# Kernel optimization log

Hardware: AMD Instinct MI355X
Metric: run time of the kernel (lower is better)

## Reference

```python
import jax, jax.numpy as jnp
import numpy as np

B, D, H, M, N, S = 256, 256, 512, 64, 2048, 3
SHIFTS = (1, 0, -1)  # = range(S//2, -S//2, -1); matches np.roll(eye, s, axis=1) one-hot matrices


def setup_inputs():
    key = jax.random.key(0)
    k = jax.random.split(key, 24)
    f32 = jnp.float32

    def rn(i, shape, scale):
        return jax.random.normal(k[i], shape, f32) * scale

    rh = jax.random.uniform(k[3], (B, N), f32)
    wh = jax.random.uniform(k[4], (B, N), f32)
    sc_ih = 1.0 / np.sqrt(D + M)
    sc_h = 1.0 / np.sqrt(H)
    return dict(
        inp=rn(0, (B, D), 1.0),
        h_tm1=rn(1, (B, H), 0.1),
        c_tm1=rn(2, (B, H), 0.1),
        read_head_tm1=rh / rh.sum(1, keepdims=True),
        write_head_tm1=wh / wh.sum(1, keepdims=True),
        memory=rn(5, (B, N, M), 0.5),
        W_ih=rn(6, (4 * H, D + M), sc_ih), W_hh=rn(7, (4 * H, H), sc_h),
        b_ih=jnp.zeros((4 * H,), f32), b_hh=jnp.zeros((4 * H,), f32),
        W_rk=rn(8, (M, H), sc_h), b_rk=rn(9, (M,), 0.01),
        W_wk=rn(10, (M, H), sc_h), b_wk=rn(11, (M,), 0.01),
        W_rc=rn(12, (3, H), sc_h), b_rc=jnp.zeros((3,), f32),
        W_wc=rn(13, (3, H), sc_h), b_wc=jnp.zeros((3,), f32),
        W_rs=rn(14, (S, H), sc_h), b_rs=jnp.zeros((S,), f32),
        W_ws=rn(15, (S, H), sc_h), b_ws=jnp.zeros((S,), f32),
        W_w=rn(16, (2 * M, H), sc_h), b_w=jnp.zeros((2 * M,), f32),
    )


def _head_params(h, Wk, bk, Wc, bc, Ws, bs):
    kk = jnp.tanh(h @ Wk.T + bk)                     # [B,M] key
    c = h @ Wc.T + bc                                # [B,3]
    beta = jax.nn.relu(c[:, 0:1]) + 1e-4             # focus strength
    g = jax.nn.sigmoid(c[:, 1:2])                    # interpolation gate
    gamma = jax.nn.relu(c[:, 2:3]) + 1.0001          # sharpening power
    s = jax.nn.softmax(h @ Ws.T + bs, axis=1)        # [B,S] shift weights
    return kk, s, beta, g, gamma


def _address(memory, head_tm1, kk, s, beta, g, gamma):
    dot = jnp.einsum('bm,bnm->bn', kk, memory)
    nk = jnp.linalg.norm(kk, axis=1, keepdims=True)  # [B,1]
    nM = jnp.linalg.norm(memory, axis=2)             # [B,N]
    cos = dot / jnp.maximum(nk * nM, 1e-8)
    content = jax.nn.softmax(beta * cos, axis=1)
    inter = g * content + (1.0 - g) * head_tm1       # gated interpolation [B,N]
    # circular shift; identical math to contracting with the one-hot C tensor
    rolled = jnp.stack([jnp.roll(inter, -sh, axis=1) for sh in SHIFTS], axis=1)  # [B,S,N]
    out = jnp.einsum('bsn,bs->bn', rolled, s)
    out = out ** gamma                               # sharpen
    return out / out.sum(1, keepdims=True)


def reference(inp, h_tm1, c_tm1, read_head_tm1, write_head_tm1, memory,
              W_ih, W_hh, b_ih, b_hh, W_rk, b_rk, W_wk, b_wk,
              W_rc, b_rc, W_wc, b_wc, W_rs, b_rs, W_ws, b_ws, W_w, b_w):
    # read addressing uses previous hidden state
    rp = _head_params(h_tm1, W_rk, b_rk, W_rc, b_rc, W_rs, b_rs)
    read_head = _address(memory, read_head_tm1, *rp)
    M_read = jnp.einsum('bn,bnm->bm', read_head, memory)  # [B,M]
    # LSTMCell controller (torch gate order i,f,g,o)
    x = jnp.concatenate([inp, M_read], axis=1)
    z = x @ W_ih.T + b_ih + h_tm1 @ W_hh.T + b_hh
    zi, zf, zg, zo = jnp.split(z, 4, axis=1)
    c_t = jax.nn.sigmoid(zf) * c_tm1 + jax.nn.sigmoid(zi) * jnp.tanh(zg)
    h_t = jax.nn.sigmoid(zo) * jnp.tanh(c_t)
    # write addressing uses new hidden state
    wp = _head_params(h_t, W_wk, b_wk, W_wc, b_wc, W_ws, b_ws)
    write_head = _address(memory, write_head_tm1, *wp)
    wa = h_t @ W_w.T + b_w
    e = jax.nn.sigmoid(wa[:, :M])                    # erase
    a = jnp.tanh(wa[:, M:])                          # add
    ww = write_head[:, :, None]                      # [B,N,1]
    M_out = memory * (1.0 - ww * e[:, None, :]) + ww * a[:, None, :]
    return (h_t, c_t, read_head, write_head, M_out)
```

## Files before the change

### kernel.cpp

```cpp
#include <hip/hip_runtime.h>
#include <hip/hip_bf16.h>

#define Bb 256
#define Dd 256
#define Hh 512
#define Mm 64
#define Nn 2048

typedef __attribute__((ext_vector_type(8))) short bf16x8;
typedef __attribute__((ext_vector_type(4))) float f32x4;

static __device__ __forceinline__ short f2bf(float f) {
    unsigned u = __float_as_uint(f);
    unsigned r = (u + 0x7FFFu + ((u >> 16) & 1u)) >> 16;
    return (short)r;
}

__global__ __launch_bounds__(256) void head_params_kernel(
    const float* __restrict__ h,
    const float* __restrict__ Wk, const float* __restrict__ bk,
    const float* __restrict__ Wc, const float* __restrict__ bc,
    const float* __restrict__ Ws, const float* __restrict__ bs,
    float* __restrict__ kk, float* __restrict__ par)
{
    int b = blockIdx.x;
    __shared__ float hs[Hh];
    __shared__ float red[6];
    __shared__ float skk[Mm];
    const float* hb = h + (size_t)b * Hh;
    for (int i = threadIdx.x; i < Hh; i += 256) hs[i] = hb[i];
    __syncthreads();

    int m   = threadIdx.x >> 2;
    int sub = threadIdx.x & 3;
    {
        const float* w = Wk + (size_t)m * Hh + sub * 128;
        const float* hh = hs + sub * 128;
        float acc = 0.f;
        #pragma unroll 8
        for (int k = 0; k < 128; ++k) acc += hh[k] * w[k];
        acc += __shfl_xor(acc, 1, 64);
        acc += __shfl_xor(acc, 2, 64);
        if (sub == 0) {
            float v = tanhf(acc + bk[m]);
            kk[(size_t)b * Mm + m] = v;
            skk[m] = v;
        }
    }
    if (threadIdx.x < 24) {
        int o  = threadIdx.x >> 2;
        int su = threadIdx.x & 3;
        const float* w = ((o < 3) ? (Wc + (size_t)o * Hh) : (Ws + (size_t)(o - 3) * Hh)) + su * 128;
        const float* hh = hs + su * 128;
        float acc = 0.f;
        #pragma unroll 8
        for (int k = 0; k < 128; ++k) acc += hh[k] * w[k];
        acc += __shfl_xor(acc, 1, 64);
        acc += __shfl_xor(acc, 2, 64);
        if (su == 0) red[o] = acc + ((o < 3) ? bc[o] : bs[o - 3]);
    }
    __syncthreads();
    if (threadIdx.x == 0) {
        float beta  = fmaxf(red[0], 0.f) + 1e-4f;
        float g     = 1.f / (1.f + __expf(-red[1]));
        float gamma = fmaxf(red[2], 0.f) + 1.0001f;
        float l0 = red[3], l1 = red[4], l2 = red[5];
        float mx = fmaxf(l0, fmaxf(l1, l2));
        float e0 = __expf(l0 - mx), e1 = __expf(l1 - mx), e2 = __expf(l2 - mx);
        float inv = 1.f / (e0 + e1 + e2);
        float ssq = 0.f;
        #pragma unroll
        for (int i = 0; i < Mm; ++i) ssq += skk[i] * skk[i];
        float* p = par + (size_t)b * 8;
        p[0] = beta; p[1] = g; p[2] = gamma;
        p[3] = e0 * inv; p[4] = e1 * inv; p[5] = e2 * inv;
        p[6] = sqrtf(ssq);
    }
}

__global__ __launch_bounds__(1024) void wparams_wvec_kernel(
    const float* __restrict__ h,
    const float* __restrict__ Wk, const float* __restrict__ bk,
    const float* __restrict__ Wc, const float* __restrict__ bc,
    const float* __restrict__ Ws, const float* __restrict__ bs,
    const float* __restrict__ W_w, const float* __restrict__ b_w,
    float* __restrict__ kk, float* __restrict__ par, float* __restrict__ ea)
{
    int b = blockIdx.x;
    int t = threadIdx.x;
    __shared__ float hs[Hh];
    __shared__ float red6[6];
    __shared__ float skk[Mm];
    if (t < Hh) hs[t] = h[(size_t)b * Hh + t];
    __syncthreads();
    if (t < 256) {
        int m = t >> 2, sub = t & 3;
        const float* w = Wk + (size_t)m * Hh + sub * 128;
        const float* hh = hs + sub * 128;
        float acc = 0.f;
        #pragma unroll 8
        for (int k = 0; k < 128; ++k) acc += hh[k] * w[k];
        acc += __shfl_xor(acc, 1, 64);
        acc += __shfl_xor(acc, 2, 64);
        if (sub == 0) {
            float v = tanhf(acc + bk[m]);
            skk[m] = v;
            kk[(size_t)b * Mm + m] = v;
        }
    } else if (t < 280) {
        int o = (t - 256) >> 2, su = t & 3;
        const float* w = ((o < 3) ? (Wc + (size_t)o * Hh) : (Ws + (size_t)(o - 3) * Hh)) + su * 128;
        const float* hh = hs + su * 128;
        float acc = 0.f;
        #pragma unroll 8
        for (int k = 0; k < 128; ++k) acc += hh[k] * w[k];
        acc += __shfl_xor(acc, 1, 64);
        acc += __shfl_xor(acc, 2, 64);
        if (su == 0) red6[o] = acc + ((o < 3) ? bc[o] : bs[o - 3]);
    } else if (t >= 512) {
        int o = (t - 512) >> 2, su = t & 3;
        const float* w = W_w + (size_t)o * Hh + su * 128;
        const float* hh = hs + su * 128;
        float acc = 0.f;
        #pragma unroll 8
        for (int k = 0; k < 128; ++k) acc += hh[k] * w[k];
        acc += __shfl_xor(acc, 1, 64);
        acc += __shfl_xor(acc, 2, 64);
        if (su == 0) {
            float v = acc + b_w[o];
            ea[(size_t)b * 128 + o] = (o < Mm) ? (1.f / (1.f + __expf(-v))) : tanhf(v);
        }
    }
    __syncthreads();
    if (t < 64) {
        float v = skk[t];
        float ssq = v * v;
        #pragma unroll
        for (int msk = 1; msk < 64; msk <<= 1) ssq += __shfl_xor(ssq, msk, 64);
        if (t == 0) {
            float beta  = fmaxf(red6[0], 0.f) + 1e-4f;
            float g     = 1.f / (1.f + __expf(-red6[1]));
            float gamma = fmaxf(red6[2], 0.f) + 1.0001f;
            float l0 = red6[3], l1 = red6[4], l2 = red6[5];
            float mx = fmaxf(l0, fmaxf(l1, l2));
            float e0 = __expf(l0 - mx), e1 = __expf(l1 - mx), e2 = __expf(l2 - mx);
            float inv = 1.f / (e0 + e1 + e2);
            float* p = par + (size_t)b * 8;
            p[0] = beta; p[1] = g; p[2] = gamma;
            p[3] = e0 * inv; p[4] = e1 * inv; p[5] = e2 * inv;
            p[6] = sqrtf(ssq);
        }
    }
}

template <int COMPUTE_NORM>
__global__ __launch_bounds__(256) void cos_pass_kernel(
    const float* __restrict__ mem, const float* __restrict__ kk,
    const float* __restrict__ par, float* __restrict__ cosv,
    float* __restrict__ nM)
{
    int b  = blockIdx.x >> 3;
    int n0 = (blockIdx.x & 7) << 8;
    int w  = threadIdx.x >> 6;
    int l  = threadIdx.x & 63;
    int m4 = l & 15;
    int rq = l >> 4;

    float4 kv = ((const float4*)(kk + (size_t)b * Mm))[m4];
    float kn = par[(size_t)b * 8 + 6];
    const float4* mb4 = (const float4*)(mem + (size_t)b * Nn * Mm);

    #pragma unroll
    for (int q = 0; q < 16; ++q) {
        int n = n0 + w * 64 + q * 4 + rq;
        size_t row = (size_t)b * Nn + n;
        float4 v = mb4[(size_t)n * 16 + m4];
        float dot = v.x * kv.x + v.y * kv.y + v.z * kv.z + v.w * kv.w;
        dot += __shfl_xor(dot, 1, 64);
        dot += __shfl_xor(dot, 2, 64);
        dot += __shfl_xor(dot, 4, 64);
        dot += __shfl_xor(dot, 8, 64);
        if (COMPUTE_NORM) {
            float ss = v.x * v.x + v.y * v.y + v.z * v.z + v.w * v.w;
            ss += __shfl_xor(ss, 1, 64);
            ss += __shfl_xor(ss, 2, 64);
            ss += __shfl_xor(ss, 4, 64);
            ss += __shfl_xor(ss, 8, 64);
            if (m4 == 0) {
                float nm = sqrtf(ss);
                nM[row] = nm;
                cosv[row] = dot / fmaxf(kn * nm, 1e-8f);
            }
        } else {
            if (m4 == 0) {
                float nm = nM[row];
                cosv[row] = dot / fmaxf(kn * nm, 1e-8f);
            }
        }
    }
}

__global__ __launch_bounds__(1024) void raddr_mread_kernel(
    const float* __restrict__ cosv, const float* __restrict__ par,
    const float* __restrict__ prev, const float* __restrict__ mem,
    float* __restrict__ outh, float* __restrict__ mrd)
{
    int b = blockIdx.x;
    int t = threadIdx.x;
    int w = t >> 6, l = t & 63;
    __shared__ float csh[Nn];
    __shared__ float redw[16];
    __shared__ float4 red4[64][16];

    const float* pv = par + (size_t)b * 8;
    float beta = pv[0], g = pv[1], gamma = pv[2];
    float s0 = pv[3], s1 = pv[4], s2 = pv[5];

    float v0 = beta * cosv[(size_t)b * Nn + t];
    float v1 = beta * cosv[(size_t)b * Nn + t + 1024];
    float mx = fmaxf(v0, v1);
    #pragma unroll
    for (int msk = 1; msk < 64; msk <<= 1) mx = fmaxf(mx, __shfl_xor(mx, msk, 64));
    if (l == 0) redw[w] = mx;
    __syncthreads();
    mx = redw[0];
    #pragma unroll
    for (int i = 1; i < 16; ++i) mx = fmaxf(mx, redw[i]);
    float e0 = __expf(v0 - mx), e1 = __expf(v1 - mx);
    float sum = e0 + e1;
    #pragma unroll
    for (int msk = 1; msk < 64; msk <<= 1) sum += __shfl_xor(sum, msk, 64);
    __syncthreads();
    if (l == 0) redw[w] = sum;
    __syncthreads();
    sum = 0.f;
    #pragma unroll
    for (int i = 0; i < 16; ++i) sum += redw[i];
    float invs = 1.f / sum;
    const float* pb = prev + (size_t)b * Nn;
    float i0 = g * e0 * invs + (1.f - g) * pb[t];
    float i1 = g * e1 * invs + (1.f - g) * pb[t + 1024];
    csh[t] = i0; csh[t + 1024] = i1;
    __syncthreads();
    int n1 = t + 1024;
    float c0 = s0 * csh[(t + 1) & (Nn - 1)] + s1 * i0 + s2 * csh[(t - 1) & (Nn - 1)];
    float c1 = s0 * csh[(n1 + 1) & (Nn - 1)] + s1 * i1 + s2 * csh[(n1 - 1) & (Nn - 1)];
    float p0 = exp2f(gamma * __log2f(c0));
    float p1 = exp2f(gamma * __log2f(c1));
    float osum = p0 + p1;
    #pragma unroll
    for (int msk = 1; msk < 64; msk <<= 1) osum += __shfl_xor(osum, msk, 64);
    __syncthreads();
    if (l == 0) redw[w] = osum;
    __syncthreads();
    osum = 0.f;
    #pragma unroll
    for (int i = 0; i < 16; ++i) osum += redw[i];
    float inv2 = 1.f / osum;
    float h0 = p0 * inv2, h1 = p1 * inv2;
    outh[(size_t)b * Nn + t] = h0;
    outh[(size_t)b * Nn + n1] = h1;
    __syncthreads();
    csh[t] = h0; csh[n1] = h1;
    __syncthreads();

    int r = t >> 4;
    int c = t & 15;
    const float4* mb4 = (const float4*)(mem + (size_t)b * Nn * Mm);
    float ax = 0.f, ay = 0.f, az = 0.f, aw = 0.f;
    for (int n = r; n < Nn; n += 64) {
        float wgt = csh[n];
        float4 v = mb4[(size_t)n * 16 + c];
        ax += wgt * v.x; ay += wgt * v.y; az += wgt * v.z; aw += wgt * v.w;
    }
    red4[r][c] = make_float4(ax, ay, az, aw);
    __syncthreads();
    if (t < 256) {
        int gg = t >> 4, cc = t & 15;
        float4 a = red4[gg * 4 + 0][cc], bq = red4[gg * 4 + 1][cc];
        float4 cv = red4[gg * 4 + 2][cc], d = red4[gg * 4 + 3][cc];
        red4[gg * 4][cc] = make_float4(a.x + bq.x + cv.x + d.x, a.y + bq.y + cv.y + d.y,
                                       a.z + bq.z + cv.z + d.z, a.w + bq.w + cv.w + d.w);
    }
    __syncthreads();
    if (t < 16) {
        float sx = 0.f, sy = 0.f, sz = 0.f, sw = 0.f;
        #pragma unroll
        for (int gg = 0; gg < 16; ++gg) {
            float4 v = red4[gg * 4][t];
            sx += v.x; sy += v.y; sz += v.z; sw += v.w;
        }
        ((float4*)(mrd + (size_t)b * Mm))[t] = make_float4(sx, sy, sz, sw);
    }
}

__global__ __launch_bounds__(256) void waddr_kernel(
    const float* __restrict__ cosv, const float* __restrict__ par,
    const float* __restrict__ prev, float* __restrict__ outh)
{
    int b = blockIdx.x;
    __shared__ float sh[Nn];
    __shared__ float red[4];
    const float* cb = cosv + (size_t)b * Nn;
    const float* pv = par + (size_t)b * 8;
    float beta = pv[0], g = pv[1], gamma = pv[2];
    float s0 = pv[3], s1 = pv[4], s2 = pv[5];
    int tid = threadIdx.x;

    float vals[8];
    float mx = -1e30f;
    #pragma unroll
    for (int i = 0; i < 8; ++i) {
        float v = beta * cb[tid + i * 256];
        vals[i] = v;
        mx = fmaxf(mx, v);
    }
    #pragma unroll
    for (int msk = 1; msk < 64; msk <<= 1) mx = fmaxf(mx, __shfl_xor(mx, msk, 64));
    if ((tid & 63) == 0) red[tid >> 6] = mx;
    __syncthreads();
    mx = fmaxf(fmaxf(red[0], red[1]), fmaxf(red[2], red[3]));

    float sum = 0.f;
    #pragma unroll
    for (int i = 0; i < 8; ++i) {
        float e = __expf(vals[i] - mx);
        vals[i] = e;
        sum += e;
    }
    #pragma unroll
    for (int msk = 1; msk < 64; msk <<= 1) sum += __shfl_xor(sum, msk, 64);
    __syncthreads();
    if ((tid & 63) == 0) red[tid >> 6] = sum;
    __syncthreads();
    sum = red[0] + red[1] + red[2] + red[3];
    float invs = 1.f / sum;

    const float* pb = prev + (size_t)b * Nn;
    #pragma unroll
    for (int i = 0; i < 8; ++i) {
        int n = tid + i * 256;
        sh[n] = g * vals[i] * invs + (1.f - g) * pb[n];
    }
    __syncthreads();

    float outs[8];
    float osum = 0.f;
    #pragma unroll
    for (int i = 0; i < 8; ++i) {
        int n = tid + i * 256;
        float v = s0 * sh[(n + 1) & (Nn - 1)] + s1 * sh[n] + s2 * sh[(n - 1) & (Nn - 1)];
        v = exp2f(gamma * __log2f(v));
        outs[i] = v;
        osum += v;
    }
    #pragma unroll
    for (int msk = 1; msk < 64; msk <<= 1) osum += __shfl_xor(osum, msk, 64);
    __syncthreads();
    if ((tid & 63) == 0) red[tid >> 6] = osum;
    __syncthreads();
    osum = red[0] + red[1] + red[2] + red[3];
    float inv2 = 1.f / osum;
    #pragma unroll
    for (int i = 0; i < 8; ++i)
        outh[(size_t)b * Nn + tid + i * 256] = outs[i] * inv2;
}

__global__ __launch_bounds__(256) void convW_kernel(
    const float* __restrict__ W_ih, const float* __restrict__ W_hh,
    short* __restrict__ Wb)
{
    unsigned g = blockIdx.x * 256 + threadIdx.x;
    unsigned j = g / 104u;
    unsigned kq = (g - j * 104u) * 8u;
    const float* src = (kq < 320u) ? (W_ih + (size_t)j * 320 + kq)
                                   : (W_hh + (size_t)j * 512 + (kq - 320u));
    float4 a = ((const float4*)src)[0];
    float4 c = ((const float4*)src)[1];
    bf16x8 o;
    o[0] = f2bf(a.x); o[1] = f2bf(a.y); o[2] = f2bf(a.z); o[3] = f2bf(a.w);
    o[4] = f2bf(c.x); o[5] = f2bf(c.y); o[6] = f2bf(c.z); o[7] = f2bf(c.w);
    *(bf16x8*)(Wb + (size_t)j * 832 + kq) = o;
}

__global__ __launch_bounds__(256) void convA_kernel(
    const float* __restrict__ inp, const float* __restrict__ mrd,
    const float* __restrict__ h, short* __restrict__ Ab)
{
    unsigned g = blockIdx.x * 256 + threadIdx.x;
    unsigned r = g / 104u;
    unsigned kq = (g - r * 104u) * 8u;
    const float* src;
    if (kq < 256u)      src = inp + (size_t)r * 256 + kq;
    else if (kq < 320u) src = mrd + (size_t)r * 64 + (kq - 256u);
    else                src = h + (size_t)r * 512 + (kq - 320u);
    float4 a = ((const float4*)src)[0];
    float4 c = ((const float4*)src)[1];
    bf16x8 o;
    o[0] = f2bf(a.x); o[1] = f2bf(a.y); o[2] = f2bf(a.z); o[3] = f2bf(a.w);
    o[4] = f2bf(c.x); o[5] = f2bf(c.y); o[6] = f2bf(c.z); o[7] = f2bf(c.w);
    *(bf16x8*)(Ab + (size_t)r * 832 + kq) = o;
}

#define LDA 56
__global__ __launch_bounds__(256) void lstm_gemm_mfma(
    const short* __restrict__ Ab, const short* __restrict__ Wb,
    const float* __restrict__ b_ih, const float* __restrict__ b_hh,
    float* __restrict__ z)
{
    __shared__ short As[64][LDA];
    __shared__ short Bs[64][LDA];
    int t = threadIdx.x;
    int r0 = blockIdx.x * 64, c0 = blockIdx.y * 64;
    int w = t >> 6, l = t & 63;
    int wr = (w >> 1) * 32, wc = (w & 1) * 32;
    int ar = t >> 2, kq = (t & 3) * 8;
    int lr = l & 15, kb = (l >> 4) * 8;

    f32x4 acc00 = {0.f, 0.f, 0.f, 0.f}, acc01 = {0.f, 0.f, 0.f, 0.f};
    f32x4 acc10 = {0.f, 0.f, 0.f, 0.f}, acc11 = {0.f, 0.f, 0.f, 0.f};

    for (int kt = 0; kt < 26; ++kt) {
        int k0 = kt * 32;
        *(bf16x8*)&As[ar][kq] = *(const bf16x8*)(Ab + (size_t)(r0 + ar) * 832 + k0 + kq);
        *(bf16x8*)&Bs[ar][kq] = *(const bf16x8*)(Wb + (size_t)(c0 + ar) * 832 + k0 + kq);
        __syncthreads();
        bf16x8 a0 = *(const bf16x8*)&As[wr + lr][kb];
        bf16x8 a1 = *(const bf16x8*)&As[wr + 16 + lr][kb];
        bf16x8 b0 = *(const bf16x8*)&Bs[wc + lr][kb];
        bf16x8 b1 = *(const bf16x8*)&Bs[wc + 16 + lr][kb];
        acc00 = __builtin_amdgcn_mfma_f32_16x16x32_bf16(a0, b0, acc00, 0, 0, 0);
        acc01 = __builtin_amdgcn_mfma_f32_16x16x32_bf16(a0, b1, acc01, 0, 0, 0);
        acc10 = __builtin_amdgcn_mfma_f32_16x16x32_bf16(a1, b0, acc10, 0, 0, 0);
        acc11 = __builtin_amdgcn_mfma_f32_16x16x32_bf16(a1, b1, acc11, 0, 0, 0);
        __syncthreads();
    }
    int rq = (l >> 4) * 4;
    #pragma unroll
    for (int q = 0; q < 4; ++q) {
        int row0 = r0 + wr + rq + q;
        int col0 = c0 + wc + lr;
        z[(size_t)row0 * 2048 + col0] = acc00[q] + b_ih[col0] + b_hh[col0];
        z[(size_t)row0 * 2048 + col0 + 16] = acc01[q] + b_ih[col0 + 16] + b_hh[col0 + 16];
        z[(size_t)(row0 + 16) * 2048 + col0] = acc10[q] + b_ih[col0] + b_hh[col0];
        z[(size_t)(row0 + 16) * 2048 + col0 + 16] = acc11[q] + b_ih[col0 + 16] + b_hh[col0 + 16];
    }
}

__global__ __launch_bounds__(256) void gates_kernel(
    const float* __restrict__ z, const float* __restrict__ c_tm1,
    float* __restrict__ h_out, float* __restrict__ c_out)
{
    int idx = blockIdx.x * 256 + threadIdx.x;
    int b = idx >> 9, hh = idx & 511;
    const float* zb = z + (size_t)b * 2048;
    float zi = zb[hh], zf = zb[512 + hh], zg = zb[1024 + hh], zo = zb[1536 + hh];
    float si = 1.f / (1.f + __expf(-zi));
    float sf = 1.f / (1.f + __expf(-zf));
    float so = 1.f / (1.f + __expf(-zo));
    float ct = sf * c_tm1[idx] + si * tanhf(zg);
    float ht = so * tanhf(ct);
    c_out[idx] = ct;
    h_out[idx] = ht;
}

__global__ __launch_bounds__(256) void mout_kernel(
    const float* __restrict__ mem, const float* __restrict__ head,
    const float* __restrict__ ea, float* __restrict__ out)
{
    const size_t total = (size_t)Bb * Nn * Mm / 4;
    for (size_t i4 = (size_t)blockIdx.x * 256 + threadIdx.x; i4 < total;
         i4 += (size_t)2048 * 256) {
        size_t row = i4 >> 4;
        int m4 = (int)(i4 & 15);
        int b = (int)(row >> 11);
        float w = head[row];
        float4 mv = ((const float4*)mem)[i4];
        const float4* e4p = (const float4*)(ea + (size_t)b * 128);
        float4 ev = e4p[m4];
        float4 av = e4p[16 + m4];
        float4 o;
        o.x = mv.x * (1.f - w * ev.x) + w * av.x;
        o.y = mv.y * (1.f - w * ev.y) + w * av.y;
        o.z = mv.z * (1.f - w * ev.z) + w * av.z;
        o.w = mv.w * (1.f - w * ev.w) + w * av.w;
        ((float4*)out)[i4] = o;
    }
}

extern "C" void kernel_launch(void* const* d_in, const int* in_sizes, int n_in,
                              void* d_out, int out_size, void* d_ws, size_t ws_size,
                              hipStream_t stream)
{
    const float* inp   = (const float*)d_in[0];
    const float* h_tm1 = (const float*)d_in[1];
    const float* c_tm1 = (const float*)d_in[2];
    const float* rh0   = (const float*)d_in[3];
    const float* wh0   = (const float*)d_in[4];
    const float* mem   = (const float*)d_in[5];
    const float* W_ih  = (const float*)d_in[6];
    const float* W_hh  = (const float*)d_in[7];
    const float* b_ih  = (const float*)d_in[8];
    const float* b_hh  = (const float*)d_in[9];
    const float* W_rk  = (const float*)d_in[10];
    const float* b_rk  = (const float*)d_in[11];
    const float* W_wk  = (const float*)d_in[12];
    const float* b_wk  = (const float*)d_in[13];
    const float* W_rc  = (const float*)d_in[14];
    const float* b_rc  = (const float*)d_in[15];
    const float* W_wc  = (const float*)d_in[16];
    const float* b_wc  = (const float*)d_in[17];
    const float* W_rs  = (const float*)d_in[18];
    const float* b_rs  = (const float*)d_in[19];
    const float* W_ws  = (const float*)d_in[20];
    const float* b_ws  = (const float*)d_in[21];
    const float* W_w   = (const float*)d_in[22];
    const float* b_w   = (const float*)d_in[23];

    float* out   = (float*)d_out;
    float* h_t   = out;
    float* c_t   = out + 131072;
    float* rhead = out + 262144;
    float* whead = out + 786432;
    float* mo    = out + 1310720;
    float* cosbuf = mo;
    float* zbuf   = mo + 524288;
    float* nMbuf  = mo + 1048576;
    short* Ab     = (short*)(mo + 1572864);
    short* Wb     = (short*)(mo + 1679360);

    float* ws  = (float*)d_ws;
    float* kk  = ws;
    float* par = ws + 16384;
    float* mrd = ws + 18432;
    float* ea  = ws + 34816;

    convW_kernel<<<832, 256, 0, stream>>>(W_ih, W_hh, Wb);

    head_params_kernel<<<Bb, 256, 0, stream>>>(h_tm1, W_rk, b_rk, W_rc, b_rc, W_rs, b_rs, kk, par);
    cos_pass_kernel<1><<<Bb * 8, 256, 0, stream>>>(mem, kk, par, cosbuf, nMbuf);
    raddr_mread_kernel<<<Bb, 1024, 0, stream>>>(cosbuf, par, rh0, mem, rhead, mrd);
    convA_kernel<<<104, 256, 0, stream>>>(inp, mrd, h_tm1, Ab);
    lstm_gemm_mfma<<<dim3(4, 32), 256, 0, stream>>>(Ab, Wb, b_ih, b_hh, zbuf);
    gates_kernel<<<Bb * Hh / 256, 256, 0, stream>>>(zbuf, c_tm1, h_t, c_t);

    wparams_wvec_kernel<<<Bb, 1024, 0, stream>>>(
        h_t, W_wk, b_wk, W_wc, b_wc, W_ws, b_ws, W_w, b_w, kk, par, ea);
    cos_pass_kernel<0><<<Bb * 8, 256, 0, stream>>>(mem, kk, par, cosbuf, nMbuf);
    waddr_kernel<<<Bb, 256, 0, stream>>>(cosbuf, par, wh0, whead);
    mout_kernel<<<2048, 256, 0, stream>>>(mem, whead, ea, mo);
}
```

Before: 166.9 us.

## Stage memory as bf16 once and fuse addressing, gate and conversion kernels

```diff
diff --git a/kernel.cpp b/kernel.cpp
--- a/kernel.cpp
+++ b/kernel.cpp
@@ -2,37 +2,54 @@
 #include <hip/hip_bf16.h>
 
 #define Bb 256
-#define Dd 256
 #define Hh 512
 #define Mm 64
 #define Nn 2048
 
 typedef __attribute__((ext_vector_type(8))) short bf16x8;
 typedef __attribute__((ext_vector_type(4))) float f32x4;
+typedef __attribute__((ext_vector_type(4))) unsigned short u16x4;
 
 static __device__ __forceinline__ short f2bf(float f) {
     unsigned u = __float_as_uint(f);
     unsigned r = (u + 0x7FFFu + ((u >> 16) & 1u)) >> 16;
     return (short)r;
 }
-
-__global__ __launch_bounds__(256) void head_params_kernel(
+static __device__ __forceinline__ float bf2f(unsigned short u) {
+    return __uint_as_float(((unsigned)u) << 16);
+}
+
+__global__ __launch_bounds__(256) void convW_headparams_kernel(
+    const float* __restrict__ W_ih, const float* __restrict__ W_hh,
+    short* __restrict__ Wb,
     const float* __restrict__ h,
     const float* __restrict__ Wk, const float* __restrict__ bk,
     const float* __restrict__ Wc, const float* __restrict__ bc,
     const float* __restrict__ Ws, const float* __restrict__ bs,
     float* __restrict__ kk, float* __restrict__ par)
 {
-    int b = blockIdx.x;
+    if (blockIdx.x < 832) {
+        unsigned g = blockIdx.x * 256 + threadIdx.x;
+        unsigned j = g / 104u;
+        unsigned kq = (g - j * 104u) * 8u;
+        const float* src = (kq < 320u) ? (W_ih + (size_t)j * 320 + kq)
+                                       : (W_hh + (size_t)j * 512 + (kq - 320u));
+        float4 a = ((const float4*)src)[0];
+        float4 c = ((const float4*)src)[1];
+        bf16x8 o;
+        o[0] = f2bf(a.x); o[1] = f2bf(a.y); o[2] = f2bf(a.z); o[3] = f2bf(a.w);
+        o[4] = f2bf(c.x); o[5] = f2bf(c.y); o[6] = f2bf(c.z); o[7] = f2bf(c.w);
+        *(bf16x8*)(Wb + (size_t)j * 832 + kq) = o;
+        return;
+    }
+    int b = blockIdx.x - 832;
     __shared__ float hs[Hh];
     __shared__ float red[6];
     __shared__ float skk[Mm];
     const float* hb = h + (size_t)b * Hh;
     for (int i = threadIdx.x; i < Hh; i += 256) hs[i] = hb[i];
     __syncthreads();
-
-    int m   = threadIdx.x >> 2;
-    int sub = threadIdx.x & 3;
+    int m = threadIdx.x >> 2, sub = threadIdx.x & 3;
     {
         const float* w = Wk + (size_t)m * Hh + sub * 128;
         const float* hh = hs + sub * 128;
@@ -48,8 +65,7 @@
         }
     }
     if (threadIdx.x < 24) {
-        int o  = threadIdx.x >> 2;
-        int su = threadIdx.x & 3;
+        int o = threadIdx.x >> 2, su = threadIdx.x & 3;
         const float* w = ((o < 3) ? (Wc + (size_t)o * Hh) : (Ws + (size_t)(o - 3) * Hh)) + su * 128;
         const float* hh = hs + su * 128;
         float acc = 0.f;
@@ -78,12 +94,213 @@
     }
 }
 
-__global__ __launch_bounds__(1024) void wparams_wvec_kernel(
-    const float* __restrict__ h,
+__global__ __launch_bounds__(256) void convM_cos_kernel(
+    const float* __restrict__ mem, const float* __restrict__ kk,
+    const float* __restrict__ par, float* __restrict__ cosv,
+    short* __restrict__ memb)
+{
+    int b  = blockIdx.x >> 3;
+    int n0 = (blockIdx.x & 7) << 8;
+    int w  = threadIdx.x >> 6;
+    int l  = threadIdx.x & 63;
+    int m4 = l & 15;
+    int rq = l >> 4;
+
+    float4 kv = ((const float4*)(kk + (size_t)b * Mm))[m4];
+    float kn = par[(size_t)b * 8 + 6];
+    const float4* mb4 = (const float4*)(mem + (size_t)b * Nn * Mm);
+    short* ob = memb + (size_t)b * Nn * Mm;
+
+    #pragma unroll
+    for (int q = 0; q < 16; ++q) {
+        int n = n0 + w * 64 + q * 4 + rq;
+        float4 v = mb4[(size_t)n * 16 + m4];
+        u16x4 o;
+        o[0] = (unsigned short)f2bf(v.x); o[1] = (unsigned short)f2bf(v.y);
+        o[2] = (unsigned short)f2bf(v.z); o[3] = (unsigned short)f2bf(v.w);
+        *(u16x4*)(ob + (size_t)n * 64 + m4 * 4) = o;
+        float dot = v.x * kv.x + v.y * kv.y + v.z * kv.z + v.w * kv.w;
+        float ss  = v.x * v.x + v.y * v.y + v.z * v.z + v.w * v.w;
+        dot += __shfl_xor(dot, 1, 64); ss += __shfl_xor(ss, 1, 64);
+        dot += __shfl_xor(dot, 2, 64); ss += __shfl_xor(ss, 2, 64);
+        dot += __shfl_xor(dot, 4, 64); ss += __shfl_xor(ss, 4, 64);
+        dot += __shfl_xor(dot, 8, 64); ss += __shfl_xor(ss, 8, 64);
+        if (m4 == 0) cosv[(size_t)b * Nn + n] = dot / fmaxf(kn * sqrtf(ss), 1e-8f);
+    }
+}
+
+__global__ __launch_bounds__(1024) void raddr_mread_convA_kernel(
+    const float* __restrict__ cosv, const float* __restrict__ par,
+    const float* __restrict__ prev, const short* __restrict__ memb,
+    const float* __restrict__ inp, const float* __restrict__ h,
+    float* __restrict__ outh, short* __restrict__ Ab)
+{
+    int b = blockIdx.x;
+    int t = threadIdx.x;
+    int w = t >> 6, l = t & 63;
+    __shared__ float csh[Nn];
+    __shared__ float redw[16];
+    __shared__ float4 red4[64][16];
+    __shared__ float mrdL[Mm];
+
+    const float* pv = par + (size_t)b * 8;
+    float beta = pv[0], g = pv[1], gamma = pv[2];
+    float s0 = pv[3], s1 = pv[4], s2 = pv[5];
+
+    float v0 = beta * cosv[(size_t)b * Nn + t];
+    float v1 = beta * cosv[(size_t)b * Nn + t + 1024];
+    float mx = fmaxf(v0, v1);
+    #pragma unroll
+    for (int msk = 1; msk < 64; msk <<= 1) mx = fmaxf(mx, __shfl_xor(mx, msk, 64));
+    if (l == 0) redw[w] = mx;
+    __syncthreads();
+    mx = redw[0];
+    #pragma unroll
+    for (int i = 1; i < 16; ++i) mx = fmaxf(mx, redw[i]);
+    float e0 = __expf(v0 - mx), e1 = __expf(v1 - mx);
+    float sum = e0 + e1;
+    #pragma unroll
+    for (int msk = 1; msk < 64; msk <<= 1) sum += __shfl_xor(sum, msk, 64);
+    __syncthreads();
+    if (l == 0) redw[w] = sum;
+    __syncthreads();
+    sum = 0.f;
+    #pragma unroll
+    for (int i = 0; i < 16; ++i) sum += redw[i];
+    float invs = 1.f / sum;
+    const float* pb = prev + (size_t)b * Nn;
+    float i0 = g * e0 * invs + (1.f - g) * pb[t];
+    float i1 = g * e1 * invs + (1.f - g) * pb[t + 1024];
+    csh[t] = i0; csh[t + 1024] = i1;
+    __syncthreads();
+    int n1 = t + 1024;
+    float c0 = s0 * csh[(t + 1) & (Nn - 1)] + s1 * i0 + s2 * csh[(t - 1) & (Nn - 1)];
+    float c1 = s0 * csh[(n1 + 1) & (Nn - 1)] + s1 * i1 + s2 * csh[(n1 - 1) & (Nn - 1)];
+    float p0 = exp2f(gamma * __log2f(c0));
+    float p1 = exp2f(gamma * __log2f(c1));
+    float osum = p0 + p1;
+    #pragma unroll
+    for (int msk = 1; msk < 64; msk <<= 1) osum += __shfl_xor(osum, msk, 64);
+    __syncthreads();
+    if (l == 0) redw[w] = osum;
+    __syncthreads();
+    osum = 0.f;
+    #pragma unroll
+    for (int i = 0; i < 16; ++i) osum += redw[i];
+    float inv2 = 1.f / osum;
+    float h0 = p0 * inv2, h1 = p1 * inv2;
+    outh[(size_t)b * Nn + t] = h0;
+    outh[(size_t)b * Nn + n1] = h1;
+    __syncthreads();
+    csh[t] = h0; csh[n1] = h1;
+    __syncthreads();
+
+    int r = t >> 4;
+    int c = t & 15;
+    const short* mb = memb + (size_t)b * Nn * Mm;
+    float ax = 0.f, ay = 0.f, az = 0.f, aw = 0.f;
+    for (int n = r; n < Nn; n += 64) {
+        float wgt = csh[n];
+        u16x4 uv = *(const u16x4*)(mb + (size_t)n * 64 + c * 4);
+        ax += wgt * bf2f(uv[0]); ay += wgt * bf2f(uv[1]);
+        az += wgt * bf2f(uv[2]); aw += wgt * bf2f(uv[3]);
+    }
+    red4[r][c] = make_float4(ax, ay, az, aw);
+    __syncthreads();
+    if (t < 256) {
+        int gg = t >> 4, cc = t & 15;
+        float4 a = red4[gg * 4 + 0][cc], bq = red4[gg * 4 + 1][cc];
+        float4 cv = red4[gg * 4 + 2][cc], d = red4[gg * 4 + 3][cc];
+        red4[gg * 4][cc] = make_float4(a.x + bq.x + cv.x + d.x, a.y + bq.y + cv.y + d.y,
+                                       a.z + bq.z + cv.z + d.z, a.w + bq.w + cv.w + d.w);
+    }
+    __syncthreads();
+    if (t < 16) {
+        float sx = 0.f, sy = 0.f, sz = 0.f, sw = 0.f;
+        #pragma unroll
+        for (int gg = 0; gg < 16; ++gg) {
+            float4 v = red4[gg * 4][t];
+            sx += v.x; sy += v.y; sz += v.z; sw += v.w;
+        }
+        mrdL[t * 4 + 0] = sx; mrdL[t * 4 + 1] = sy;
+        mrdL[t * 4 + 2] = sz; mrdL[t * 4 + 3] = sw;
+    }
+    __syncthreads();
+
+    if (t < 104) {
+        int kq = t * 8;
+        float v[8];
+        if (kq < 256) {
+            const float* s = inp + (size_t)b * 256 + kq;
+            #pragma unroll
+            for (int i = 0; i < 8; ++i) v[i] = s[i];
+        } else if (kq < 320) {
+            #pragma unroll
+            for (int i = 0; i < 8; ++i) v[i] = mrdL[kq - 256 + i];
+        } else {
+            const float* s = h + (size_t)b * 512 + (kq - 320);
+            #pragma unroll
+            for (int i = 0; i < 8; ++i) v[i] = s[i];
+        }
+        bf16x8 o;
+        #pragma unroll
+        for (int i = 0; i < 8; ++i) o[i] = f2bf(v[i]);
+        *(bf16x8*)(Ab + (size_t)b * 832 + kq) = o;
+    }
+}
+
+#define LDA 56
+__global__ __launch_bounds__(256) void lstm_gemm_mfma(
+    const short* __restrict__ Ab, const short* __restrict__ Wb,
+    const float* __restrict__ b_ih, const float* __restrict__ b_hh,
+    float* __restrict__ z)
+{
+    __shared__ short As[64][LDA];
+    __shared__ short Bs[64][LDA];
+    int t = threadIdx.x;
+    int r0 = blockIdx.x * 64, c0 = blockIdx.y * 64;
+    int w = t >> 6, l = t & 63;
+    int wr = (w >> 1) * 32, wc = (w & 1) * 32;
+    int ar = t >> 2, kq = (t & 3) * 8;
+    int lr = l & 15, kb = (l >> 4) * 8;
+
+    f32x4 acc00 = {0.f, 0.f, 0.f, 0.f}, acc01 = {0.f, 0.f, 0.f, 0.f};
+    f32x4 acc10 = {0.f, 0.f, 0.f, 0.f}, acc11 = {0.f, 0.f, 0.f, 0.f};
+
+    for (int kt = 0; kt < 26; ++kt) {
+        int k0 = kt * 32;
+        *(bf16x8*)&As[ar][kq] = *(const bf16x8*)(Ab + (size_t)(r0 + ar) * 832 + k0 + kq);
+        *(bf16x8*)&Bs[ar][kq] = *(const bf16x8*)(Wb + (size_t)(c0 + ar) * 832 + k0 + kq);
+        __syncthreads();
+        bf16x8 a0 = *(const bf16x8*)&As[wr + lr][kb];
+        bf16x8 a1 = *(const bf16x8*)&As[wr + 16 + lr][kb];
+        bf16x8 b0 = *(const bf16x8*)&Bs[wc + lr][kb];
+        bf16x8 b1 = *(const bf16x8*)&Bs[wc + 16 + lr][kb];
+        acc00 = __builtin_amdgcn_mfma_f32_16x16x32_bf16(a0, b0, acc00, 0, 0, 0);
+        acc01 = __builtin_amdgcn_mfma_f32_16x16x32_bf16(a0, b1, acc01, 0, 0, 0);
+        acc10 = __builtin_amdgcn_mfma_f32_16x16x32_bf16(a1, b0, acc10, 0, 0, 0);
+        acc11 = __builtin_amdgcn_mfma_f32_16x16x32_bf16(a1, b1, acc11, 0, 0, 0);
+        __syncthreads();
+    }
+    int rq = (l >> 4) * 4;
+    #pragma unroll
+    for (int q = 0; q < 4; ++q) {
+        int row0 = r0 + wr + rq + q;
+        int col0 = c0 + wc + lr;
+        z[(size_t)row0 * 2048 + col0] = acc00[q] + b_ih[col0] + b_hh[col0];
+        z[(size_t)row0 * 2048 + col0 + 16] = acc01[q] + b_ih[col0 + 16] + b_hh[col0 + 16];
+        z[(size_t)(row0 + 16) * 2048 + col0] = acc10[q] + b_ih[col0] + b_hh[col0];
+        z[(size_t)(row0 + 16) * 2048 + col0 + 16] = acc11[q] + b_ih[col0 + 16] + b_hh[col0 + 16];
+    }
+}
+
+__global__ __launch_bounds__(1024) void gates_wparams_kernel(
+    const float* __restrict__ z, const float* __restrict__ c_tm1,
     const float* __restrict__ Wk, const float* __restrict__ bk,
     const float* __restrict__ Wc, const float* __restrict__ bc,
     const float* __restrict__ Ws, const float* __restrict__ bs,
     const float* __restrict__ W_w, const float* __restrict__ b_w,
+    float* __restrict__ h_out, float* __restrict__ c_out,
     float* __restrict__ kk, float* __restrict__ par, float* __restrict__ ea)
 {
     int b = blockIdx.x;
@@ -91,8 +308,21 @@
     __shared__ float hs[Hh];
     __shared__ float red6[6];
     __shared__ float skk[Mm];
-    if (t < Hh) hs[t] = h[(size_t)b * Hh + t];
-    __syncthreads();
+
+    if (t < 512) {
+        const float* zb = z + (size_t)b * 2048;
+        float zi = zb[t], zf = zb[512 + t], zg = zb[1024 + t], zo = zb[1536 + t];
+        float si = 1.f / (1.f + __expf(-zi));
+        float sf = 1.f / (1.f + __expf(-zf));
+        float so = 1.f / (1.f + __expf(-zo));
+        float ct = sf * c_tm1[(size_t)b * 512 + t] + si * tanhf(zg);
+        float ht = so * tanhf(ct);
+        c_out[(size_t)b * 512 + t] = ct;
+        h_out[(size_t)b * 512 + t] = ht;
+        hs[t] = ht;
+    }
+    __syncthreads();
+
     if (t < 256) {
         int m = t >> 2, sub = t & 3;
         const float* w = Wk + (size_t)m * Hh + sub * 128;
@@ -153,71 +383,41 @@
     }
 }
 
-template <int COMPUTE_NORM>
-__global__ __launch_bounds__(256) void cos_pass_kernel(
-    const float* __restrict__ mem, const float* __restrict__ kk,
-    const float* __restrict__ par, float* __restrict__ cosv,
-    float* __restrict__ nM)
-{
-    int b  = blockIdx.x >> 3;
-    int n0 = (blockIdx.x & 7) << 8;
-    int w  = threadIdx.x >> 6;
-    int l  = threadIdx.x & 63;
-    int m4 = l & 15;
-    int rq = l >> 4;
-
-    float4 kv = ((const float4*)(kk + (size_t)b * Mm))[m4];
-    float kn = par[(size_t)b * 8 + 6];
-    const float4* mb4 = (const float4*)(mem + (size_t)b * Nn * Mm);
-
-    #pragma unroll
-    for (int q = 0; q < 16; ++q) {
-        int n = n0 + w * 64 + q * 4 + rq;
-        size_t row = (size_t)b * Nn + n;
-        float4 v = mb4[(size_t)n * 16 + m4];
-        float dot = v.x * kv.x + v.y * kv.y + v.z * kv.z + v.w * kv.w;
-        dot += __shfl_xor(dot, 1, 64);
-        dot += __shfl_xor(dot, 2, 64);
-        dot += __shfl_xor(dot, 4, 64);
-        dot += __shfl_xor(dot, 8, 64);
-        if (COMPUTE_NORM) {
-            float ss = v.x * v.x + v.y * v.y + v.z * v.z + v.w * v.w;
-            ss += __shfl_xor(ss, 1, 64);
-            ss += __shfl_xor(ss, 2, 64);
-            ss += __shfl_xor(ss, 4, 64);
-            ss += __shfl_xor(ss, 8, 64);
-            if (m4 == 0) {
-                float nm = sqrtf(ss);
-                nM[row] = nm;
-                cosv[row] = dot / fmaxf(kn * nm, 1e-8f);
-            }
-        } else {
-            if (m4 == 0) {
-                float nm = nM[row];
-                cosv[row] = dot / fmaxf(kn * nm, 1e-8f);
-            }
-        }
-    }
-}
-
-__global__ __launch_bounds__(1024) void raddr_mread_kernel(
-    const float* __restrict__ cosv, const float* __restrict__ par,
-    const float* __restrict__ prev, const float* __restrict__ mem,
-    float* __restrict__ outh, float* __restrict__ mrd)
+__global__ __launch_bounds__(1024) void wfused_kernel(
+    const short* __restrict__ memb, const float* __restrict__ kk,
+    const float* __restrict__ par, const float* __restrict__ prev,
+    float* __restrict__ outh)
 {
     int b = blockIdx.x;
     int t = threadIdx.x;
     int w = t >> 6, l = t & 63;
+    int m4 = l & 15, rq = l >> 4;
     __shared__ float csh[Nn];
     __shared__ float redw[16];
-    __shared__ float4 red4[64][16];
 
     const float* pv = par + (size_t)b * 8;
+    float kn = pv[6];
     float beta = pv[0], g = pv[1], gamma = pv[2];
     float s0 = pv[3], s1 = pv[4], s2 = pv[5];
-
-    float v0 = beta * cosv[(size_t)b * Nn + t];
-    float v1 = beta * cosv[(size_t)b * Nn + t + 1024];
+    float4 kv = ((const float4*)(kk + (size_t)b * Mm))[m4];
+    const short* mb = memb + (size_t)b * Nn * Mm;
+
+    #pragma unroll 4
+    for (int it = 0; it < 32; ++it) {
+        int n = it * 64 + w * 4 + rq;
+        u16x4 uv = *(const u16x4*)(mb + (size_t)n * 64 + m4 * 4);
+        float x0 = bf2f(uv[0]), x1 = bf2f(uv[1]), x2 = bf2f(uv[2]), x3 = bf2f(uv[3]);
+        float dot = x0 * kv.x + x1 * kv.y + x2 * kv.z + x3 * kv.w;
+        float ss  = x0 * x0 + x1 * x1 + x2 * x2 + x3 * x3;
+        dot += __shfl_xor(dot, 1, 64); ss += __shfl_xor(ss, 1, 64);
+        dot += __shfl_xor(dot, 2, 64); ss += __shfl_xor(ss, 2, 64);
+        dot += __shfl_xor(dot, 4, 64); ss += __shfl_xor(ss, 4, 64);
+        dot += __shfl_xor(dot, 8, 64); ss += __shfl_xor(ss, 8, 64);
+        if (m4 == 0) csh[n] = dot / fmaxf(kn * sqrtf(ss), 1e-8f);
+    }
+    __syncthreads();
+
+    float v0 = beta * csh[t], v1 = beta * csh[t + 1024];
     float mx = fmaxf(v0, v1);
     #pragma unroll
     for (int msk = 1; msk < 64; msk <<= 1) mx = fmaxf(mx, __shfl_xor(mx, msk, 64));
@@ -240,6 +440,7 @@
     const float* pb = prev + (size_t)b * Nn;
     float i0 = g * e0 * invs + (1.f - g) * pb[t];
     float i1 = g * e1 * invs + (1.f - g) * pb[t + 1024];
+    __syncthreads();
     csh[t] = i0; csh[t + 1024] = i1;
     __syncthreads();
     int n1 = t + 1024;
@@ -257,216 +458,15 @@
     #pragma unroll
     for (int i = 0; i < 16; ++i) osum += redw[i];
     float inv2 = 1.f / osum;
-    float h0 = p0 * inv2, h1 = p1 * inv2;
-    outh[(size_t)b * Nn + t] = h0;
-    outh[(size_t)b * Nn + n1] = h1;
-    __syncthreads();
-    csh[t] = h0; csh[n1] = h1;
-    __syncthreads();
-
-    int r = t >> 4;
-    int c = t & 15;
-    const float4* mb4 = (const float4*)(mem + (size_t)b * Nn * Mm);
-    float ax = 0.f, ay = 0.f, az = 0.f, aw = 0.f;
-    for (int n = r; n < Nn; n += 64) {
-        float wgt = csh[n];
-        float4 v = mb4[(size_t)n * 16 + c];
-        ax += wgt * v.x; ay += wgt * v.y; az += wgt * v.z; aw += wgt * v.w;
-    }
-    red4[r][c] = make_float4(ax, ay, az, aw);
-    __syncthreads();
-    if (t < 256) {
-        int gg = t >> 4, cc = t & 15;
-        float4 a = red4[gg * 4 + 0][cc], bq = red4[gg * 4 + 1][cc];
-        float4 cv = red4[gg * 4 + 2][cc], d = red4[gg * 4 + 3][cc];
-        red4[gg * 4][cc] = make_float4(a.x + bq.x + cv.x + d.x, a.y + bq.y + cv.y + d.y,
-                                       a.z + bq.z + cv.z + d.z, a.w + bq.w + cv.w + d.w);
-    }
-    __syncthreads();
-    if (t < 16) {
-        float sx = 0.f, sy = 0.f, sz = 0.f, sw = 0.f;
-        #pragma unroll
-        for (int gg = 0; gg < 16; ++gg) {
-            float4 v = red4[gg * 4][t];
-            sx += v.x; sy += v.y; sz += v.z; sw += v.w;
-        }
-        ((float4*)(mrd + (size_t)b * Mm))[t] = make_float4(sx, sy, sz, sw);
-    }
-}
-
-__global__ __launch_bounds__(256) void waddr_kernel(
-    const float* __restrict__ cosv, const float* __restrict__ par,
-    const float* __restrict__ prev, float* __restrict__ outh)
-{
-    int b = blockIdx.x;
-    __shared__ float sh[Nn];
-    __shared__ float red[4];
-    const float* cb = cosv + (size_t)b * Nn;
-    const float* pv = par + (size_t)b * 8;
-    float beta = pv[0], g = pv[1], gamma = pv[2];
-    float s0 = pv[3], s1 = pv[4], s2 = pv[5];
-    int tid = threadIdx.x;
-
-    float vals[8];
-    float mx = -1e30f;
-    #pragma unroll
-    for (int i = 0; i < 8; ++i) {
-        float v = beta * cb[tid + i * 256];
-        vals[i] = v;
-        mx = fmaxf(mx, v);
-    }
-    #pragma unroll
-    for (int msk = 1; msk < 64; msk <<= 1) mx = fmaxf(mx, __shfl_xor(mx, msk, 64));
-    if ((tid & 63) == 0) red[tid >> 6] = mx;
-    __syncthreads();
-    mx = fmaxf(fmaxf(red[0], red[1]), fmaxf(red[2], red[3]));
-
-    float sum = 0.f;
-    #pragma unroll
-    for (int i = 0; i < 8; ++i) {
-        float e = __expf(vals[i] - mx);
-        vals[i] = e;
-        sum += e;
-    }
-    #pragma unroll
-    for (int msk = 1; msk < 64; msk <<= 1) sum += __shfl_xor(sum, msk, 64);
-    __syncthreads();
-    if ((tid & 63) == 0) red[tid >> 6] = sum;
-    __syncthreads();
-    sum = red[0] + red[1] + red[2] + red[3];
-    float invs = 1.f / sum;
-
-    const float* pb = prev + (size_t)b * Nn;
-    #pragma unroll
-    for (int i = 0; i < 8; ++i) {
-        int n = tid + i * 256;
-        sh[n] = g * vals[i] * invs + (1.f - g) * pb[n];
-    }
-    __syncthreads();
-
-    float outs[8];
-    float osum = 0.f;
-    #pragma unroll
-    for (int i = 0; i < 8; ++i) {
-        int n = tid + i * 256;
-        float v = s0 * sh[(n + 1) & (Nn - 1)] + s1 * sh[n] + s2 * sh[(n - 1) & (Nn - 1)];
-        v = exp2f(gamma * __log2f(v));
-        outs[i] = v;
-        osum += v;
-    }
-    #pragma unroll
-    for (int msk = 1; msk < 64; msk <<= 1) osum += __shfl_xor(osum, msk, 64);
-    __syncthreads();
-    if ((tid & 63) == 0) red[tid >> 6] = osum;
-    __syncthreads();
-    osum = red[0] + red[1] + red[2] + red[3];
-    float inv2 = 1.f / osum;
-    #pragma unroll
-    for (int i = 0; i < 8; ++i)
-        outh[(size_t)b * Nn + tid + i * 256] = outs[i] * inv2;
-}
-
-__global__ __launch_bounds__(256) void convW_kernel(
-    const float* __restrict__ W_ih, const float* __restrict__ W_hh,
-    short* __restrict__ Wb)
-{
-    unsigned g = blockIdx.x * 256 + threadIdx.x;
-    unsigned j = g / 104u;
-    unsigned kq = (g - j * 104u) * 8u;
-    const float* src = (kq < 320u) ? (W_ih + (size_t)j * 320 + kq)
-                                   : (W_hh + (size_t)j * 512 + (kq - 320u));
-    float4 a = ((const float4*)src)[0];
-    float4 c = ((const float4*)src)[1];
-    bf16x8 o;
-    o[0] = f2bf(a.x); o[1] = f2bf(a.y); o[2] = f2bf(a.z); o[3] = f2bf(a.w);
-    o[4] = f2bf(c.x); o[5] = f2bf(c.y); o[6] = f2bf(c.z); o[7] = f2bf(c.w);
-    *(bf16x8*)(Wb + (size_t)j * 832 + kq) = o;
-}
-
-__global__ __launch_bounds__(256) void convA_kernel(
-    const float* __restrict__ inp, const float* __restrict__ mrd,
-    const float* __restrict__ h, short* __restrict__ Ab)
-{
-    unsigned g = blockIdx.x * 256 + threadIdx.x;
-    unsigned r = g / 104u;
-    unsigned kq = (g - r * 104u) * 8u;
-    const float* src;
-    if (kq < 256u)      src = inp + (size_t)r * 256 + kq;
-    else if (kq < 320u) src = mrd + (size_t)r * 64 + (kq - 256u);
-    else                src = h + (size_t)r * 512 + (kq - 320u);
-    float4 a = ((const float4*)src)[0];
-    float4 c = ((const float4*)src)[1];
-    bf16x8 o;
-    o[0] = f2bf(a.x); o[1] = f2bf(a.y); o[2] = f2bf(a.z); o[3] = f2bf(a.w);
-    o[4] = f2bf(c.x); o[5] = f2bf(c.y); o[6] = f2bf(c.z); o[7] = f2bf(c.w);
-    *(bf16x8*)(Ab + (size_t)r * 832 + kq) = o;
-}
-
-#define LDA 56
-__global__ __launch_bounds__(256) void lstm_gemm_mfma(
-    const short* __restrict__ Ab, const short* __restrict__ Wb,
-    const float* __restrict__ b_ih, const float* __restrict__ b_hh,
-    float* __restrict__ z)
-{
-    __shared__ short As[64][LDA];
-    __shared__ short Bs[64][LDA];
-    int t = threadIdx.x;
-    int r0 = blockIdx.x * 64, c0 = blockIdx.y * 64;
-    int w = t >> 6, l = t & 63;
-    int wr = (w >> 1) * 32, wc = (w & 1) * 32;
-    int ar = t >> 2, kq = (t & 3) * 8;
-    int lr = l & 15, kb = (l >> 4) * 8;
-
-    f32x4 acc00 = {0.f, 0.f, 0.f, 0.f}, acc01 = {0.f, 0.f, 0.f, 0.f};
-    f32x4 acc10 = {0.f, 0.f, 0.f, 0.f}, acc11 = {0.f, 0.f, 0.f, 0.f};
-
-    for (int kt = 0; kt < 26; ++kt) {
-        int k0 = kt * 32;
-        *(bf16x8*)&As[ar][kq] = *(const bf16x8*)(Ab + (size_t)(r0 + ar) * 832 + k0 + kq);
-        *(bf16x8*)&Bs[ar][kq] = *(const bf16x8*)(Wb + (size_t)(c0 + ar) * 832 + k0 + kq);
-        __syncthreads();
-        bf16x8 a0 = *(const bf16x8*)&As[wr + lr][kb];
-        bf16x8 a1 = *(const bf16x8*)&As[wr + 16 + lr][kb];
-        bf16x8 b0 = *(const bf16x8*)&Bs[wc + lr][kb];
-        bf16x8 b1 = *(const bf16x8*)&Bs[wc + 16 + lr][kb];
-        acc00 = __builtin_amdgcn_mfma_f32_16x16x32_bf16(a0, b0, acc00, 0, 0, 0);
-        acc01 = __builtin_amdgcn_mfma_f32_16x16x32_bf16(a0, b1, acc01, 0, 0, 0);
-        acc10 = __builtin_amdgcn_mfma_f32_16x16x32_bf16(a1, b0, acc10, 0, 0, 0);
-        acc11 = __builtin_amdgcn_mfma_f32_16x16x32_bf16(a1, b1, acc11, 0, 0, 0);
-        __syncthreads();
-    }
-    int rq = (l >> 4) * 4;
-    #pragma unroll
-    for (int q = 0; q < 4; ++q) {
-        int row0 = r0 + wr + rq + q;
-        int col0 = c0 + wc + lr;
-        z[(size_t)row0 * 2048 + col0] = acc00[q] + b_ih[col0] + b_hh[col0];
-        z[(size_t)row0 * 2048 + col0 + 16] = acc01[q] + b_ih[col0 + 16] + b_hh[col0 + 16];
-        z[(size_t)(row0 + 16) * 2048 + col0] = acc10[q] + b_ih[col0] + b_hh[col0];
-        z[(size_t)(row0 + 16) * 2048 + col0 + 16] = acc11[q] + b_ih[col0 + 16] + b_hh[col0 + 16];
-    }
-}
-
-__global__ __launch_bounds__(256) void gates_kernel(
-    const float* __restrict__ z, const float* __restrict__ c_tm1,
-    float* __restrict__ h_out, float* __restrict__ c_out)
-{
-    int idx = blockIdx.x * 256 + threadIdx.x;
-    int b = idx >> 9, hh = idx & 511;
-    const float* zb = z + (size_t)b * 2048;
-    float zi = zb[hh], zf = zb[512 + hh], zg = zb[1024 + hh], zo = zb[1536 + hh];
-    float si = 1.f / (1.f + __expf(-zi));
-    float sf = 1.f / (1.f + __expf(-zf));
-    float so = 1.f / (1.f + __expf(-zo));
-    float ct = sf * c_tm1[idx] + si * tanhf(zg);
-    float ht = so * tanhf(ct);
-    c_out[idx] = ct;
-    h_out[idx] = ht;
-}
-
+    outh[(size_t)b * Nn + t] = p0 * inv2;
+    outh[(size_t)b * Nn + n1] = p1 * inv2;
+}
+
+template <int BF16SRC>
 __global__ __launch_bounds__(256) void mout_kernel(
-    const float* __restrict__ mem, const float* __restrict__ head,
-    const float* __restrict__ ea, float* __restrict__ out)
+    const float* __restrict__ mem, const short* __restrict__ memb,
+    const float* __restrict__ head, const float* __restrict__ ea,
+    float* __restrict__ out)
 {
     const size_t total = (size_t)Bb * Nn * Mm / 4;
     for (size_t i4 = (size_t)blockIdx.x * 256 + threadIdx.x; i4 < total;
@@ -475,7 +475,13 @@
         int m4 = (int)(i4 & 15);
         int b = (int)(row >> 11);
         float w = head[row];
-        float4 mv = ((const float4*)mem)[i4];
+        float4 mv;
+        if (BF16SRC) {
+            u16x4 uv = ((const u16x4*)memb)[i4];
+            mv = make_float4(bf2f(uv[0]), bf2f(uv[1]), bf2f(uv[2]), bf2f(uv[3]));
+        } else {
+            mv = ((const float4*)mem)[i4];
+        }
         const float4* e4p = (const float4*)(ea + (size_t)b * 128);
         float4 ev = e4p[m4];
         float4 av = e4p[16 + m4];
@@ -525,28 +531,31 @@
     float* mo    = out + 1310720;
     float* cosbuf = mo;
     float* zbuf   = mo + 524288;
-    float* nMbuf  = mo + 1048576;
-    short* Ab     = (short*)(mo + 1572864);
-    short* Wb     = (short*)(mo + 1679360);
+    short* Ab     = (short*)(mo + 1048576);
+    short* Wb     = (short*)(mo + 1179648);
 
     float* ws  = (float*)d_ws;
     float* kk  = ws;
     float* par = ws + 16384;
-    float* mrd = ws + 18432;
-    float* ea  = ws + 34816;
-
-    convW_kernel<<<832, 256, 0, stream>>>(W_ih, W_hh, Wb);
-
-    head_params_kernel<<<Bb, 256, 0, stream>>>(h_tm1, W_rk, b_rk, W_rc, b_rc, W_rs, b_rs, kk, par);
-    cos_pass_kernel<1><<<Bb * 8, 256, 0, stream>>>(mem, kk, par, cosbuf, nMbuf);
-    raddr_mread_kernel<<<Bb, 1024, 0, stream>>>(cosbuf, par, rh0, mem, rhead, mrd);
-    convA_kernel<<<104, 256, 0, stream>>>(inp, mrd, h_tm1, Ab);
+    float* ea  = ws + 18432;
+
+    const size_t memb_elems = (size_t)Bb * Nn * Mm;
+    const bool big_ws = ws_size >= (size_t)51200 * 4 + memb_elems * 2;
+    short* memb = big_ws ? (short*)(ws + 51200)
+                         : (short*)(mo + 2097152);
+
+    convW_headparams_kernel<<<1088, 256, 0, stream>>>(
+        W_ih, W_hh, Wb, h_tm1, W_rk, b_rk, W_rc, b_rc, W_rs, b_rs, kk, par);
+    convM_cos_kernel<<<2048, 256, 0, stream>>>(mem, kk, par, cosbuf, memb);
+    raddr_mread_convA_kernel<<<Bb, 1024, 0, stream>>>(
+        cosbuf, par, rh0, memb, inp, h_tm1, rhead, Ab);
     lstm_gemm_mfma<<<dim3(4, 32), 256, 0, stream>>>(Ab, Wb, b_ih, b_hh, zbuf);
-    gates_kernel<<<Bb * Hh / 256, 256, 0, stream>>>(zbuf, c_tm1, h_t, c_t);
-
-    wparams_wvec_kernel<<<Bb, 1024, 0, stream>>>(
-        h_t, W_wk, b_wk, W_wc, b_wc, W_ws, b_ws, W_w, b_w, kk, par, ea);
-    cos_pass_kernel<0><<<Bb * 8, 256, 0, stream>>>(mem, kk, par, cosbuf, nMbuf);
-    waddr_kernel<<<Bb, 256, 0, stream>>>(cosbuf, par, wh0, whead);
-    mout_kernel<<<2048, 256, 0, stream>>>(mem, whead, ea, mo);
-}
+    gates_wparams_kernel<<<Bb, 1024, 0, stream>>>(
+        zbuf, c_tm1, W_wk, b_wk, W_wc, b_wc, W_ws, b_ws, W_w, b_w,
+        h_t, c_t, kk, par, ea);
+    wfused_kernel<<<Bb, 1024, 0, stream>>>(memb, kk, par, wh0, whead);
+    if (big_ws)
+        mout_kernel<1><<<2048, 256, 0, stream>>>(mem, memb, whead, ea, mo);
+    else
+        mout_kernel<0><<<2048, 256, 0, stream>>>(mem, memb, whead, ea, mo);
+}
```

New measurement: 163.5 us. 1.02x faster.
